# Performance work log

Hardware: AMD Instinct MI355X
Metric: run time of the kernel (lower is better)

## Reference

```python
import jax, jax.numpy as jnp
import numpy as np

B, T, D, F, E, K = 8, 2048, 512, 2048, 16, 2  # batch, seq, d_model, d_ff, n_experts, top_k


def setup_inputs() -> dict:
    key = jax.random.key(0)
    k_x, k_r, k_w1, k_w2 = jax.random.split(key, 4)
    he = lambda k, shape, fan_in: jax.random.normal(k, shape, jnp.float32) * np.float32(np.sqrt(2.0 / fan_in))
    return {
        "x": jax.random.normal(k_x, (B, T, D), jnp.float32),
        # router: xavier_uniform approximated with matching-variance normal
        "Wr": jax.random.normal(k_r, (D, E), jnp.float32) * np.float32(np.sqrt(2.0 / (D + E))),
        "W1": he(k_w1, (E, D, F), D),   # expert first Dense kernels, he_normal
        "b1": jnp.zeros((E, F), jnp.float32),
        "W2": he(k_w2, (E, F, D), F),   # expert second Dense kernels
        "b2": jnp.zeros((E, D), jnp.float32),
    }


def reference(x, Wr, W1, b1, W2, b2):
    # ---- Router ----
    logits = jnp.einsum('btd,de->bte', x, Wr)                 # (B,T,E)
    probs = jax.nn.softmax(logits, axis=-1)
    top_v, top_i = jax.lax.top_k(logits, K)                   # (B,T,K)
    gates = jax.nn.softmax(top_v, axis=-1)                    # (B,T,K)
    # load-balancing aux loss (top-1 dispatch fraction vs mean prob)
    f = jnp.mean(jax.nn.one_hot(top_i[..., 0], E, dtype=probs.dtype), axis=(0, 1))
    P = jnp.mean(probs, axis=(0, 1))
    aux_loss = E * jnp.sum(f * P)
    # ---- All-experts FFN (as in reference: compute every expert on every token) ----
    h = jax.nn.gelu(jnp.einsum('btd,edf->ebtf', x, W1) + b1[:, None, None, :])  # (E,B,T,F)
    eo = jnp.einsum('ebtf,efd->ebtd', h, W2) + b2[:, None, None, :]             # (E,B,T,D)
    # ---- Top-k gather + combine ----
    eo_btED = jnp.transpose(eo, (1, 2, 0, 3))                 # (B,T,E,D)
    idx = top_i[..., None]                                     # (B,T,K,1)
    selected = jnp.take_along_axis(eo_btED, idx, axis=2)      # (B,T,K,D)
    output = jnp.sum(gates[..., None] * selected, axis=2)     # (B,T,D)
    # Dropout with deterministic=True is identity
    return output, aux_loss
```

## Files before the change

kernel.cpp:

```cpp
#include <hip/hip_runtime.h>
#include <cstdint>
#include <cstddef>

#define NB 8
#define TT 2048
#define DD 512
#define FF 2048
#define NE 16
#define NT (NB*TT)
#define NPOS (NT*2)
#define MT_MAX (NPOS/128 + NE)
#define NPAL (MT_MAX*128)

typedef short v8s __attribute__((ext_vector_type(8)));
typedef float v4f __attribute__((ext_vector_type(4)));

__device__ __forceinline__ uint16_t f2bf(float v) {
  union { float f; uint32_t u; } c; c.f = v;
  uint32_t r = (c.u + 0x7FFFu + ((c.u >> 16) & 1u)) >> 16;
  return (uint16_t)r;
}
__device__ __forceinline__ float bf2f(uint16_t b) {
  union { uint32_t u; float f; } c; c.u = ((uint32_t)b) << 16;
  return c.f;
}
__device__ __forceinline__ float gelu_t(float x) {
  float u = 0.7978845608028654f * (x + 0.044715f * x * x * x);
  return 0.5f * x * (1.0f + tanhf(u));
}
__device__ __forceinline__ void gl_lds16(const void* g, void* l) {
  __builtin_amdgcn_global_load_lds(
      (const __attribute__((address_space(1))) uint32_t*)g,
      (__attribute__((address_space(3))) uint32_t*)l, 16, 0, 0);
}

__global__ void k_zero(int* p, int n) {
  for (int i = threadIdx.x; i < n; i += 256) p[i] = 0;
}

__global__ __launch_bounds__(256) void k_cvt_x(const float* __restrict__ x,
                                               uint16_t* __restrict__ xb) {
  int i = (blockIdx.x * 256 + threadIdx.x) * 4;
  const float4 v = *(const float4*)(x + i);
  ushort4 o; o.x = f2bf(v.x); o.y = f2bf(v.y); o.z = f2bf(v.z); o.w = f2bf(v.w);
  *(ushort4*)(xb + i) = o;
}

__global__ __launch_bounds__(256) void k_trans(const float* __restrict__ src,
                                               uint16_t* __restrict__ dst,
                                               int rows, int cols) {
  __shared__ float t[32][33];
  const size_t eo = (size_t)blockIdx.z * rows * cols;
  const float* s = src + eo;
  uint16_t* d = dst + eo;
  int c0 = blockIdx.x * 32, r0 = blockIdx.y * 32;
  int tx = threadIdx.x, ty = threadIdx.y;
#pragma unroll
  for (int i = 0; i < 4; ++i)
    t[ty + i * 8][tx] = s[(size_t)(r0 + ty + i * 8) * cols + c0 + tx];
  __syncthreads();
#pragma unroll
  for (int i = 0; i < 4; ++i)
    d[(size_t)(c0 + ty + i * 8) * rows + r0 + tx] = f2bf(t[tx][ty + i * 8]);
}

__global__ __launch_bounds__(256) void k_router(
    const float* __restrict__ x, const float* __restrict__ Wr,
    int* __restrict__ topi, float* __restrict__ gates,
    int* __restrict__ cnt_part, int* __restrict__ f_part, float* __restrict__ P_part) {
  __shared__ int s_cnt[NE]; __shared__ int s_f[NE]; __shared__ float s_P[NE];
  const int tid = threadIdx.x;
  if (tid < NE) { s_cnt[tid] = 0; s_f[tid] = 0; s_P[tid] = 0.f; }
  __syncthreads();
  const int wid = tid >> 6, lane = tid & 63;
  const int t = blockIdx.x * 4 + wid;
  const float* xr = x + (size_t)t * DD + lane * 8;
  double pe[NE];
#pragma unroll
  for (int e = 0; e < NE; ++e) pe[e] = 0.0;
#pragma unroll
  for (int j = 0; j < 8; ++j) {
    const double xv = (double)xr[j];
    const float* wr = Wr + (size_t)(lane * 8 + j) * NE;
#pragma unroll
    for (int e = 0; e < NE; ++e) pe[e] += xv * (double)wr[e];
  }
#pragma unroll
  for (int m = 1; m < 64; m <<= 1) {
#pragma unroll
    for (int e = 0; e < NE; ++e) pe[e] += __shfl_xor(pe[e], m, 64);
  }
  if (lane == 0) {
    double mx = pe[0];
#pragma unroll
    for (int e = 1; e < NE; ++e) mx = fmax(mx, pe[e]);
    double s = 0.0, pr[NE];
#pragma unroll
    for (int e = 0; e < NE; ++e) { pr[e] = exp(pe[e] - mx); s += pr[e]; }
    const double inv = 1.0 / s;
    int i0 = 0; double v0 = pe[0];
#pragma unroll
    for (int e = 1; e < NE; ++e) if (pe[e] > v0) { v0 = pe[e]; i0 = e; }
    int i1 = -1; double v1 = -1.0e300;
#pragma unroll
    for (int e = 0; e < NE; ++e) if (e != i0 && pe[e] > v1) { v1 = pe[e]; i1 = e; }
    const double g0 = 1.0 / (1.0 + exp(v1 - v0));
    topi[t * 2] = i0; topi[t * 2 + 1] = i1;
    gates[t * 2] = (float)g0; gates[t * 2 + 1] = (float)(1.0 - g0);
    atomicAdd(&s_cnt[i0], 1); atomicAdd(&s_cnt[i1], 1);
    atomicAdd(&s_f[i0], 1);
#pragma unroll
    for (int e = 0; e < NE; ++e) atomicAdd(&s_P[e], (float)(pr[e] * inv));
  }
  __syncthreads();
  if (tid < NE) {
    const int slot = (blockIdx.x & 63) * NE + tid;
    if (s_cnt[tid]) atomicAdd(&cnt_part[slot], s_cnt[tid]);
    if (s_f[tid]) atomicAdd(&f_part[slot], s_f[tid]);
    atomicAdd(&P_part[slot], s_P[tid]);
  }
}

__global__ __launch_bounds__(256) void k_reduce(
    const int* __restrict__ cnt_part, const int* __restrict__ f_part,
    const float* __restrict__ P_part, int* __restrict__ counts,
    int* __restrict__ goff, int* __restrict__ cursor,
    int* __restrict__ tokofp, float* __restrict__ aux_out) {
  __shared__ int sc[NE]; __shared__ int sgo[NE + 1]; __shared__ double sterm[NE];
  const int tid = threadIdx.x;
  if (tid < NE) {
    int c = 0, f = 0; float P = 0.f;
    for (int s = 0; s < 64; ++s) {
      c += cnt_part[s * NE + tid]; f += f_part[s * NE + tid]; P += P_part[s * NE + tid];
    }
    counts[tid] = c; sc[tid] = c;
    sterm[tid] = ((double)f / NT) * ((double)P / NT);
  }
  __syncthreads();
  if (tid == 0) {
    double a = 0;
    for (int e = 0; e < NE; ++e) a += sterm[e];
    *aux_out = (float)(NE * a);
    int o = 0; sgo[0] = 0;
    for (int e = 0; e < NE; ++e) { o += ((sc[e] + 127) >> 7) << 7; sgo[e + 1] = o; }
    for (int e = 0; e <= NE; ++e) goff[e] = sgo[e];
    for (int e = 0; e < NE; ++e) cursor[e] = sgo[e];
  }
  __syncthreads();
  for (int e = 0; e < NE; ++e) {
    const int st = sgo[e] + sc[e], en = sgo[e + 1];
    for (int i = st + tid; i < en; i += 256) tokofp[i] = 0;
  }
}

__global__ __launch_bounds__(256) void k_build(const int* __restrict__ topi,
                                               int* __restrict__ cursor,
                                               int* __restrict__ tokofp,
                                               int* __restrict__ pos) {
  __shared__ int scnt[NE]; __shared__ int sbase[NE];
  const int tid = threadIdx.x;
  const int t = blockIdx.x * 256 + tid;
  if (tid < NE) scnt[tid] = 0;
  __syncthreads();
  const int e0 = topi[t * 2], e1 = topi[t * 2 + 1];
  const int r0 = atomicAdd(&scnt[e0], 1);
  const int r1 = atomicAdd(&scnt[e1], 1);
  __syncthreads();
  if (tid < NE) sbase[tid] = scnt[tid] ? atomicAdd(&cursor[tid], scnt[tid]) : 0;
  __syncthreads();
  const int p0 = sbase[e0] + r0, p1 = sbase[e1] + r1;
  tokofp[p0] = t; tokofp[p1] = t;
  pos[t * 2] = p0; pos[t * 2 + 1] = p1;
}

template <int KDIM, int NDIM, bool GATHER_GELU>
__global__ __launch_bounds__(256) void k_gemm(
    const uint16_t* __restrict__ Abase, const uint16_t* __restrict__ Bt,
    const float* __restrict__ bias, uint16_t* __restrict__ Cout,
    const int* __restrict__ goff, const int* __restrict__ tokofp) {
  __shared__ __align__(16) uint16_t As[128 * 64];
  __shared__ __align__(16) uint16_t Bs[128 * 64];
  const int gy = blockIdx.y;
  if (gy >= (goff[NE] >> 7)) return;
  int e = 0;
#pragma unroll
  for (int i = 1; i < NE; ++i) if (gy >= (goff[i] >> 7)) e = i;
  const int row0 = gy << 7;
  const int n0 = blockIdx.x << 7;
  const int tid = threadIdx.x, wid = tid >> 6, lane = tid & 63;

  const uint16_t* aptr[4]; const uint16_t* bptr[4];
  uint16_t* asml[4]; uint16_t* bsml[4];
  const uint16_t* Be = Bt + (size_t)e * ((size_t)NDIM * KDIM);
#pragma unroll
  for (int i = 0; i < 4; ++i) {
    const int chunk = i * 4 + wid;
    const int row = chunk * 8 + (lane >> 3);
    const int kb = ((lane & 7) << 4) ^ ((row & 7) << 4);
    const int ks = kb >> 1;
    asml[i] = &As[chunk * 512];
    bsml[i] = &Bs[chunk * 512];
    size_t arow;
    if (GATHER_GELU) arow = (size_t)tokofp[row0 + row] * KDIM;
    else             arow = (size_t)(row0 + row) * KDIM;
    aptr[i] = Abase + arow + ks;
    bptr[i] = Be + (size_t)(n0 + row) * KDIM + ks;
  }

  const int wm = wid >> 1, wn = wid & 1;
  int aoff[4][2], boff[4][2];
#pragma unroll
  for (int f = 0; f < 4; ++f) {
    const int ra = wm * 64 + f * 16 + (lane & 15);
    const int rb = wn * 64 + f * 16 + (lane & 15);
#pragma unroll
    for (int kk = 0; kk < 2; ++kk) {
      const int kb = kk * 64 + ((lane >> 4) << 4);
      aoff[f][kk] = ra * 128 + (kb ^ ((ra & 7) << 4));
      boff[f][kk] = rb * 128 + (kb ^ ((rb & 7) << 4));
    }
  }

  v4f acc[4][4];
#pragma unroll
  for (int i = 0; i < 4; ++i)
#pragma unroll
    for (int j = 0; j < 4; ++j) acc[i][j] = (v4f){0.f, 0.f, 0.f, 0.f};

  const int nkt = KDIM / 64;
  for (int kt = 0; kt < nkt; ++kt) {
#pragma unroll
    for (int i = 0; i < 4; ++i) gl_lds16(aptr[i] + kt * 64, asml[i]);
#pragma unroll
    for (int i = 0; i < 4; ++i) gl_lds16(bptr[i] + kt * 64, bsml[i]);
    __syncthreads();
#pragma unroll
    for (int kk = 0; kk < 2; ++kk) {
      v8s af[4], bfr[4];
#pragma unroll
      for (int f = 0; f < 4; ++f) af[f] = *(const v8s*)((const char*)As + aoff[f][kk]);
#pragma unroll
      for (int f = 0; f < 4; ++f) bfr[f] = *(const v8s*)((const char*)Bs + boff[f][kk]);
#pragma unroll
      for (int fm = 0; fm < 4; ++fm)
#pragma unroll
        for (int fn = 0; fn < 4; ++fn)
          acc[fm][fn] = __builtin_amdgcn_mfma_f32_16x16x32_bf16(af[fm], bfr[fn], acc[fm][fn], 0, 0, 0);
    }
    __syncthreads();
  }

#pragma unroll
  for (int fn = 0; fn < 4; ++fn) {
    const int col = n0 + wn * 64 + fn * 16 + (lane & 15);
    const float bv = bias[e * NDIM + col];
#pragma unroll
    for (int fm = 0; fm < 4; ++fm) {
      const int rb = row0 + wm * 64 + fm * 16 + ((lane >> 4) << 2);
#pragma unroll
      for (int j = 0; j < 4; ++j) {
        float v = acc[fm][fn][j] + bv;
        if (GATHER_GELU) v = gelu_t(v);
        Cout[(size_t)(rb + j) * NDIM + col] = f2bf(v);
      }
    }
  }
}

__global__ __launch_bounds__(256) void k_comb(const uint16_t* __restrict__ ybuf,
                                              const int* __restrict__ pos,
                                              const float* __restrict__ gates,
                                              float* __restrict__ out) {
  const int t = blockIdx.x;
  const int d = threadIdx.x * 2;
  const float g0 = gates[t * 2], g1 = gates[t * 2 + 1];
  const uint32_t u0 = *(const uint32_t*)(ybuf + (size_t)pos[t * 2] * DD + d);
  const uint32_t u1 = *(const uint32_t*)(ybuf + (size_t)pos[t * 2 + 1] * DD + d);
  const float o0 = g0 * bf2f((uint16_t)u0) + g1 * bf2f((uint16_t)u1);
  const float o1 = g0 * bf2f((uint16_t)(u0 >> 16)) + g1 * bf2f((uint16_t)(u1 >> 16));
  *(float2*)(out + (size_t)t * DD + d) = make_float2(o0, o1);
}

extern "C" void kernel_launch(void* const* d_in, const int* in_sizes, int n_in,
                              void* d_out, int out_size, void* d_ws, size_t ws_size,
                              hipStream_t stream) {
  const float* x  = (const float*)d_in[0];
  const float* Wr = (const float*)d_in[1];
  const float* W1 = (const float*)d_in[2];
  const float* b1 = (const float*)d_in[3];
  const float* W2 = (const float*)d_in[4];
  const float* b2 = (const float*)d_in[5];
  float* out = (float*)d_out;

  char* ws = (char*)d_ws;
  size_t o = 0;
  auto alloc = [&](size_t bytes) { size_t r = o; o += (bytes + 255) & ~(size_t)255; return r; };
  uint16_t* xb    = (uint16_t*)(ws + alloc((size_t)NT * DD * 2));
  uint16_t* W1T   = (uint16_t*)(ws + alloc((size_t)NE * FF * DD * 2));
  uint16_t* W2T   = (uint16_t*)(ws + alloc((size_t)NE * DD * FF * 2));
  uint16_t* h     = (uint16_t*)(ws + alloc((size_t)NPAL * FF * 2));
  uint16_t* ybuf  = (uint16_t*)(ws + alloc((size_t)NPAL * DD * 2));
  int*   cnt_part = (int*)(ws + alloc(64 * NE * 4));
  int*   f_part   = (int*)(ws + alloc(64 * NE * 4));
  float* P_part   = (float*)(ws + alloc(64 * NE * 4));
  int*   topi     = (int*)(ws + alloc((size_t)NT * 2 * 4));
  float* gatesb   = (float*)(ws + alloc((size_t)NT * 2 * 4));
  int*   pos      = (int*)(ws + alloc((size_t)NT * 2 * 4));
  int*   tokofp   = (int*)(ws + alloc((size_t)NPAL * 4));
  int*   counts   = (int*)(ws + alloc(NE * 4));
  int*   goff     = (int*)(ws + alloc((NE + 1) * 4));
  int*   cursor   = (int*)(ws + alloc(NE * 4));
  (void)ws_size; (void)in_sizes; (void)n_in; (void)out_size; (void)counts;

  k_zero<<<1, 256, 0, stream>>>(cnt_part, 3 * 64 * NE);
  k_cvt_x<<<NT * DD / 1024, 256, 0, stream>>>(x, xb);
  k_trans<<<dim3(FF / 32, DD / 32, NE), dim3(32, 8), 0, stream>>>(W1, W1T, DD, FF);
  k_trans<<<dim3(DD / 32, FF / 32, NE), dim3(32, 8), 0, stream>>>(W2, W2T, FF, DD);
  k_router<<<NT / 4, 256, 0, stream>>>(x, Wr, topi, gatesb, cnt_part, f_part, P_part);
  k_reduce<<<1, 256, 0, stream>>>(cnt_part, f_part, P_part, counts, goff, cursor,
                                  tokofp, out + (size_t)NT * DD);
  k_build<<<NT / 256, 256, 0, stream>>>(topi, cursor, tokofp, pos);
  k_gemm<DD, FF, true><<<dim3(FF / 128, MT_MAX), 256, 0, stream>>>(xb, W1T, b1, h, goff, tokofp);
  k_gemm<FF, DD, false><<<dim3(DD / 128, MT_MAX), 256, 0, stream>>>(h, W2T, b2, ybuf, goff, tokofp);
  k_comb<<<NT, 256, 0, stream>>>(ybuf, pos, gatesb, out);
}
```

Baseline: 624.5 us.

## Double-buffer expert GEMMs, enlarge first GEMM tile, fuse x conversion into router

Templates the grouped expert GEMM on tile size and thread count. It adds double-buffered LDS so the next K-tile's global-to-LDS loads are issued while the current tile computes. The first GEMM now uses 256x256 tiles with 512 threads, and expert groups are padded to 256 rows to match. The separate x-to-bf16 conversion kernel is folded into the router, which already reads x. ybuf is aliased onto the xb/W1T workspace region, which is no longer read when the second GEMM runs. In exchange, padding waste rises and LDS use and register pressure go up.

Result: no change. 634.0 us (+1.5%).

```diff
diff --git a/kernel.cpp b/kernel.cpp
--- a/kernel.cpp
+++ b/kernel.cpp
@@ -9,8 +9,9 @@
 #define NE 16
 #define NT (NB*TT)
 #define NPOS (NT*2)
-#define MT_MAX (NPOS/128 + NE)
-#define NPAL (MT_MAX*128)
+#define MT256 (NPOS/256 + NE)
+#define NPAL (MT256*256)
+#define MT128 (NPAL/128)
 
 typedef short v8s __attribute__((ext_vector_type(8)));
 typedef float v4f __attribute__((ext_vector_type(4)));
@@ -36,14 +37,6 @@
 
 __global__ void k_zero(int* p, int n) {
   for (int i = threadIdx.x; i < n; i += 256) p[i] = 0;
-}
-
-__global__ __launch_bounds__(256) void k_cvt_x(const float* __restrict__ x,
-                                               uint16_t* __restrict__ xb) {
-  int i = (blockIdx.x * 256 + threadIdx.x) * 4;
-  const float4 v = *(const float4*)(x + i);
-  ushort4 o; o.x = f2bf(v.x); o.y = f2bf(v.y); o.z = f2bf(v.z); o.w = f2bf(v.w);
-  *(ushort4*)(xb + i) = o;
 }
 
 __global__ __launch_bounds__(256) void k_trans(const float* __restrict__ src,
@@ -66,6 +59,7 @@
 
 __global__ __launch_bounds__(256) void k_router(
     const float* __restrict__ x, const float* __restrict__ Wr,
+    uint16_t* __restrict__ xb,
     int* __restrict__ topi, float* __restrict__ gates,
     int* __restrict__ cnt_part, int* __restrict__ f_part, float* __restrict__ P_part) {
   __shared__ int s_cnt[NE]; __shared__ int s_f[NE]; __shared__ float s_P[NE];
@@ -78,12 +72,22 @@
   double pe[NE];
 #pragma unroll
   for (int e = 0; e < NE; ++e) pe[e] = 0.0;
+  float xv8[8];
+#pragma unroll
+  for (int j = 0; j < 8; ++j) xv8[j] = xr[j];
 #pragma unroll
   for (int j = 0; j < 8; ++j) {
-    const double xv = (double)xr[j];
+    const double xv = (double)xv8[j];
     const float* wr = Wr + (size_t)(lane * 8 + j) * NE;
 #pragma unroll
     for (int e = 0; e < NE; ++e) pe[e] += xv * (double)wr[e];
+  }
+  {
+    ushort4 o0, o1;
+    o0.x = f2bf(xv8[0]); o0.y = f2bf(xv8[1]); o0.z = f2bf(xv8[2]); o0.w = f2bf(xv8[3]);
+    o1.x = f2bf(xv8[4]); o1.y = f2bf(xv8[5]); o1.z = f2bf(xv8[6]); o1.w = f2bf(xv8[7]);
+    uint16_t* xo = xb + (size_t)t * DD + lane * 8;
+    *(ushort4*)xo = o0; *(ushort4*)(xo + 4) = o1;
   }
 #pragma unroll
   for (int m = 1; m < 64; m <<= 1) {
@@ -142,7 +146,7 @@
     for (int e = 0; e < NE; ++e) a += sterm[e];
     *aux_out = (float)(NE * a);
     int o = 0; sgo[0] = 0;
-    for (int e = 0; e < NE; ++e) { o += ((sc[e] + 127) >> 7) << 7; sgo[e + 1] = o; }
+    for (int e = 0; e < NE; ++e) { o += ((sc[e] + 255) >> 8) << 8; sgo[e + 1] = o; }
     for (int e = 0; e <= NE; ++e) goff[e] = sgo[e];
     for (int e = 0; e < NE; ++e) cursor[e] = sgo[e];
   }
@@ -173,90 +177,111 @@
   pos[t * 2] = p0; pos[t * 2 + 1] = p1;
 }
 
-template <int KDIM, int NDIM, bool GATHER_GELU>
-__global__ __launch_bounds__(256) void k_gemm(
+template <int BM, int BN, int NTHR, int KDIM, int NDIM, bool GATHER_GELU>
+__global__ __launch_bounds__(NTHR, 2) void k_gemm(
     const uint16_t* __restrict__ Abase, const uint16_t* __restrict__ Bt,
     const float* __restrict__ bias, uint16_t* __restrict__ Cout,
     const int* __restrict__ goff, const int* __restrict__ tokofp) {
-  __shared__ __align__(16) uint16_t As[128 * 64];
-  __shared__ __align__(16) uint16_t Bs[128 * 64];
+  constexpr int WAVES = NTHR / 64;
+  constexpr int WN = (WAVES == 8) ? 4 : 2;
+  constexpr int WM = WAVES / WN;
+  constexpr int MF = BM / (WM * 16);
+  constexpr int NF = BN / (WN * 16);
+  constexpr int LA = BM * 64 / (NTHR * 8);
+  constexpr int LB = BN * 64 / (NTHR * 8);
+  constexpr int NKT = KDIM / 64;
+  __shared__ __align__(16) uint16_t As[2 * BM * 64];
+  __shared__ __align__(16) uint16_t Bs[2 * BN * 64];
+
+  const int ntiles = goff[NE] / BM;
   const int gy = blockIdx.y;
-  if (gy >= (goff[NE] >> 7)) return;
+  if (gy >= ntiles) return;
   int e = 0;
 #pragma unroll
-  for (int i = 1; i < NE; ++i) if (gy >= (goff[i] >> 7)) e = i;
-  const int row0 = gy << 7;
-  const int n0 = blockIdx.x << 7;
-  const int tid = threadIdx.x, wid = tid >> 6, lane = tid & 63;
-
-  const uint16_t* aptr[4]; const uint16_t* bptr[4];
-  uint16_t* asml[4]; uint16_t* bsml[4];
+  for (int i = 1; i < NE; ++i) if (gy * BM >= goff[i]) e = i;
+  const int row0 = gy * BM;
+  const int n0 = blockIdx.x * BN;
+  const int tid = threadIdx.x, lane = tid & 63;
+  const int wid = tid >> 6;
+  const int wm = wid / WN, wn = wid % WN;
+
   const uint16_t* Be = Bt + (size_t)e * ((size_t)NDIM * KDIM);
-#pragma unroll
-  for (int i = 0; i < 4; ++i) {
-    const int chunk = i * 4 + wid;
-    const int row = chunk * 8 + (lane >> 3);
-    const int kb = ((lane & 7) << 4) ^ ((row & 7) << 4);
-    const int ks = kb >> 1;
-    asml[i] = &As[chunk * 512];
-    bsml[i] = &Bs[chunk * 512];
-    size_t arow;
-    if (GATHER_GELU) arow = (size_t)tokofp[row0 + row] * KDIM;
-    else             arow = (size_t)(row0 + row) * KDIM;
-    aptr[i] = Abase + arow + ks;
-    bptr[i] = Be + (size_t)(n0 + row) * KDIM + ks;
-  }
-
-  const int wm = wid >> 1, wn = wid & 1;
-  int aoff[4][2], boff[4][2];
-#pragma unroll
-  for (int f = 0; f < 4; ++f) {
-    const int ra = wm * 64 + f * 16 + (lane & 15);
-    const int rb = wn * 64 + f * 16 + (lane & 15);
+  const uint16_t* ag[LA]; const uint16_t* bg[LB];
+  int ldsOffA[LA], ldsOffB[LB];
+#pragma unroll
+  for (int r = 0; r < LA; ++r) {
+    const int flat = r * NTHR + tid;
+    const int row = flat >> 3, slot = flat & 7;
+    ldsOffA[r] = flat * 8;
+    size_t srow;
+    if (GATHER_GELU) srow = (size_t)tokofp[row0 + row];
+    else             srow = (size_t)(row0 + row);
+    ag[r] = Abase + srow * KDIM + (slot ^ (row & 7)) * 8;
+  }
+#pragma unroll
+  for (int r = 0; r < LB; ++r) {
+    const int flat = r * NTHR + tid;
+    const int row = flat >> 3, slot = flat & 7;
+    ldsOffB[r] = flat * 8;
+    bg[r] = Be + (size_t)(n0 + row) * KDIM + (slot ^ (row & 7)) * 8;
+  }
+
+  const int kswz[2] = {
+      (((lane >> 4) << 4)) ^ ((lane & 7) << 4),
+      (64 + ((lane >> 4) << 4)) ^ ((lane & 7) << 4)};
+  const int aRow = (wm * (MF * 16) + (lane & 15)) * 128;
+  const int bRow = (wn * (NF * 16) + (lane & 15)) * 128;
+
+  v4f acc[MF][NF];
+#pragma unroll
+  for (int i = 0; i < MF; ++i)
+#pragma unroll
+    for (int j = 0; j < NF; ++j) acc[i][j] = (v4f){0.f, 0.f, 0.f, 0.f};
+
+#pragma unroll
+  for (int r = 0; r < LA; ++r) gl_lds16(ag[r], As + ldsOffA[r]);
+#pragma unroll
+  for (int r = 0; r < LB; ++r) gl_lds16(bg[r], Bs + ldsOffB[r]);
+  __syncthreads();
+
+  int cur = 0;
+  for (int kt = 0; kt < NKT; ++kt) {
+    if (kt + 1 < NKT) {
+      uint16_t* an = As + (cur ^ 1) * (BM * 64);
+      uint16_t* bn = Bs + (cur ^ 1) * (BN * 64);
+#pragma unroll
+      for (int r = 0; r < LA; ++r) gl_lds16(ag[r] + (kt + 1) * 64, an + ldsOffA[r]);
+#pragma unroll
+      for (int r = 0; r < LB; ++r) gl_lds16(bg[r] + (kt + 1) * 64, bn + ldsOffB[r]);
+    }
+    const char* ab = (const char*)(As + cur * (BM * 64));
+    const char* bb = (const char*)(Bs + cur * (BN * 64));
 #pragma unroll
     for (int kk = 0; kk < 2; ++kk) {
-      const int kb = kk * 64 + ((lane >> 4) << 4);
-      aoff[f][kk] = ra * 128 + (kb ^ ((ra & 7) << 4));
-      boff[f][kk] = rb * 128 + (kb ^ ((rb & 7) << 4));
-    }
-  }
-
-  v4f acc[4][4];
-#pragma unroll
-  for (int i = 0; i < 4; ++i)
-#pragma unroll
-    for (int j = 0; j < 4; ++j) acc[i][j] = (v4f){0.f, 0.f, 0.f, 0.f};
-
-  const int nkt = KDIM / 64;
-  for (int kt = 0; kt < nkt; ++kt) {
-#pragma unroll
-    for (int i = 0; i < 4; ++i) gl_lds16(aptr[i] + kt * 64, asml[i]);
-#pragma unroll
-    for (int i = 0; i < 4; ++i) gl_lds16(bptr[i] + kt * 64, bsml[i]);
-    __syncthreads();
-#pragma unroll
-    for (int kk = 0; kk < 2; ++kk) {
-      v8s af[4], bfr[4];
-#pragma unroll
-      for (int f = 0; f < 4; ++f) af[f] = *(const v8s*)((const char*)As + aoff[f][kk]);
-#pragma unroll
-      for (int f = 0; f < 4; ++f) bfr[f] = *(const v8s*)((const char*)Bs + boff[f][kk]);
-#pragma unroll
-      for (int fm = 0; fm < 4; ++fm)
-#pragma unroll
-        for (int fn = 0; fn < 4; ++fn)
-          acc[fm][fn] = __builtin_amdgcn_mfma_f32_16x16x32_bf16(af[fm], bfr[fn], acc[fm][fn], 0, 0, 0);
+      v8s af[MF], bf[NF];
+#pragma unroll
+      for (int f = 0; f < MF; ++f)
+        af[f] = *(const v8s*)(ab + aRow + f * 2048 + kswz[kk]);
+#pragma unroll
+      for (int f = 0; f < NF; ++f)
+        bf[f] = *(const v8s*)(bb + bRow + f * 2048 + kswz[kk]);
+#pragma unroll
+      for (int m = 0; m < MF; ++m)
+#pragma unroll
+        for (int n = 0; n < NF; ++n)
+          acc[m][n] = __builtin_amdgcn_mfma_f32_16x16x32_bf16(af[m], bf[n], acc[m][n], 0, 0, 0);
     }
     __syncthreads();
-  }
-
-#pragma unroll
-  for (int fn = 0; fn < 4; ++fn) {
-    const int col = n0 + wn * 64 + fn * 16 + (lane & 15);
+    cur ^= 1;
+  }
+
+#pragma unroll
+  for (int fn = 0; fn < NF; ++fn) {
+    const int col = n0 + wn * (NF * 16) + fn * 16 + (lane & 15);
     const float bv = bias[e * NDIM + col];
 #pragma unroll
-    for (int fm = 0; fm < 4; ++fm) {
-      const int rb = row0 + wm * 64 + fm * 16 + ((lane >> 4) << 2);
+    for (int fm = 0; fm < MF; ++fm) {
+      const int rb = row0 + wm * (MF * 16) + fm * 16 + ((lane >> 4) << 2);
 #pragma unroll
       for (int j = 0; j < 4; ++j) {
         float v = acc[fm][fn][j] + bv;
@@ -297,9 +322,9 @@
   auto alloc = [&](size_t bytes) { size_t r = o; o += (bytes + 255) & ~(size_t)255; return r; };
   uint16_t* xb    = (uint16_t*)(ws + alloc((size_t)NT * DD * 2));
   uint16_t* W1T   = (uint16_t*)(ws + alloc((size_t)NE * FF * DD * 2));
+  uint16_t* ybuf  = (uint16_t*)ws;
   uint16_t* W2T   = (uint16_t*)(ws + alloc((size_t)NE * DD * FF * 2));
   uint16_t* h     = (uint16_t*)(ws + alloc((size_t)NPAL * FF * 2));
-  uint16_t* ybuf  = (uint16_t*)(ws + alloc((size_t)NPAL * DD * 2));
   int*   cnt_part = (int*)(ws + alloc(64 * NE * 4));
   int*   f_part   = (int*)(ws + alloc(64 * NE * 4));
   float* P_part   = (float*)(ws + alloc(64 * NE * 4));
@@ -313,14 +338,15 @@
   (void)ws_size; (void)in_sizes; (void)n_in; (void)out_size; (void)counts;
 
   k_zero<<<1, 256, 0, stream>>>(cnt_part, 3 * 64 * NE);
-  k_cvt_x<<<NT * DD / 1024, 256, 0, stream>>>(x, xb);
   k_trans<<<dim3(FF / 32, DD / 32, NE), dim3(32, 8), 0, stream>>>(W1, W1T, DD, FF);
   k_trans<<<dim3(DD / 32, FF / 32, NE), dim3(32, 8), 0, stream>>>(W2, W2T, FF, DD);
-  k_router<<<NT / 4, 256, 0, stream>>>(x, Wr, topi, gatesb, cnt_part, f_part, P_part);
+  k_router<<<NT / 4, 256, 0, stream>>>(x, Wr, xb, topi, gatesb, cnt_part, f_part, P_part);
   k_reduce<<<1, 256, 0, stream>>>(cnt_part, f_part, P_part, counts, goff, cursor,
                                   tokofp, out + (size_t)NT * DD);
   k_build<<<NT / 256, 256, 0, stream>>>(topi, cursor, tokofp, pos);
-  k_gemm<DD, FF, true><<<dim3(FF / 128, MT_MAX), 256, 0, stream>>>(xb, W1T, b1, h, goff, tokofp);
-  k_gemm<FF, DD, false><<<dim3(DD / 128, MT_MAX), 256, 0, stream>>>(h, W2T, b2, ybuf, goff, tokofp);
+  k_gemm<256, 256, 512, DD, FF, true>
+      <<<dim3(FF / 256, MT256), 512, 0, stream>>>(xb, W1T, b1, h, goff, tokofp);
+  k_gemm<128, 128, 256, FF, DD, false>
+      <<<dim3(DD / 128, MT128), 256, 0, stream>>>(h, W2T, b2, ybuf, goff, tokofp);
   k_comb<<<NT, 256, 0, stream>>>(ybuf, pos, gatesb, out);
 }
```
